# Optimization experiments

Hardware: AMD Instinct MI355X
Metric: run time of the kernel (lower is better)

## Reference

```python
import jax, jax.numpy as jnp
import numpy as np

N, E, R, D = 50000, 1600000, 512, 64

def _mlp(x, w1, b1, w2, b2):
    # torch nn.Linear: y = x @ W.T + b ; Sequential(Linear(2D,D), ReLU, Linear(D,D))
    h = jax.nn.relu(x @ w1.T + b1)
    return h @ w2.T + b2

def setup_inputs() -> dict:
    key = jax.random.key(0)
    ks = jax.random.split(key, 8)
    edge_index = jax.random.randint(ks[0], (2, E), 0, N, dtype=jnp.int64)
    edge_type = jax.random.randint(ks[1], (E,), 0, R, dtype=jnp.int64)
    rel = jax.random.normal(ks[2], (R, D), dtype=jnp.float32)
    s2d = 1.0 / np.sqrt(2.0 * D)
    sd = 1.0 / np.sqrt(1.0 * D)
    w1a = jax.random.normal(ks[3], (D, 2 * D), dtype=jnp.float32) * s2d
    w2a = jax.random.normal(ks[4], (D, D), dtype=jnp.float32) * sd
    w1b = jax.random.normal(ks[5], (D, 2 * D), dtype=jnp.float32) * s2d
    w2b = jax.random.normal(ks[6], (D, D), dtype=jnp.float32) * sd
    zeros = jnp.zeros((D,), jnp.float32)
    strength = jnp.full((1,), 0.1, dtype=jnp.float32)
    return {
        'edge_index': edge_index, 'edge_type': edge_type,
        'relation_embeddings': rel,
        'w1a': w1a, 'b1a': zeros, 'w2a': w2a, 'b2a': zeros,
        'w1b': w1b, 'b1b': zeros, 'w2b': w2b, 'b2b': zeros,
        'strength': strength, 'num_nodes': N,
    }

def reference(edge_index, edge_type, relation_embeddings,
              w1a, b1a, w2a, b2a, w1b, b1b, w2b, b2b,
              strength, num_nodes):
    # Batched version of compute_entity_relation_features over all entities.
    # For entity e: feat = mean of relation embeddings over edges incident to e
    # (each edge counted once, as in the boolean-mask original).
    src, dst = edge_index[0], edge_index[1]
    rel_e = relation_embeddings[edge_type]                      # [E, D]
    not_self = (src != dst).astype(rel_e.dtype)                 # avoid double-count self-loops
    sum_feat = (jax.ops.segment_sum(rel_e, src, num_segments=num_nodes)
                + jax.ops.segment_sum(rel_e * not_self[:, None], dst, num_segments=num_nodes))
    ones = jnp.ones((rel_e.shape[0],), rel_e.dtype)
    deg = (jax.ops.segment_sum(ones, src, num_segments=num_nodes)
           + jax.ops.segment_sum(not_self, dst, num_segments=num_nodes))  # [N]
    has_edge = deg > 0
    rel_ctx = relation_embeddings.mean(axis=0)                  # [D]
    feat = jnp.where(has_edge[:, None], sum_feat / jnp.maximum(deg, 1.0)[:, None], rel_ctx)

    # interaction branch: cat(feat, global relation context) -> MLP a
    ctx_b = jnp.broadcast_to(rel_ctx, feat.shape)
    interaction = _mlp(jnp.concatenate([feat, ctx_b], axis=-1), w1a, b1a, w2a, b2a)
    # context branch: neighbor_context == entity_relation_avg == feat
    ctx_feat_n = _mlp(jnp.concatenate([feat, feat], axis=-1), w1b, b1b, w2b, b2b)
    # has_neighbor: at least one non-self-loop incident edge
    nbr_deg = (jax.ops.segment_sum(not_self, src, num_segments=num_nodes)
               + jax.ops.segment_sum(not_self, dst, num_segments=num_nodes))
    has_nbr = nbr_deg > 0
    context_feat = jnp.where(has_nbr[:, None], ctx_feat_n, interaction)

    s = jnp.clip(strength[0], 0.0, 0.3)
    enhanced = (1.0 - s) * feat + s * context_feat
    # entities with no incident edges fall back to mean relation embedding
    return jnp.where(has_edge[:, None], enhanced, rel_ctx)
```

## Files before the change

### kernel.cpp

```cpp
#include <hip/hip_runtime.h>

#define DD   64
#define WSH  6
#define WSZ  64
#define TILE 4096
#define ALGN 16
#define GMAX 1024
#define SMAX 1024
#define CAP  8192
#define LSTG 20480
#define RK   512

typedef unsigned int u32;
typedef unsigned short u16;
typedef __attribute__((ext_vector_type(4))) float f32x4;
typedef __attribute__((ext_vector_type(4))) u32 u32x4;
typedef __attribute__((ext_vector_type(8))) short short8;


__device__ inline u32 f2bf(float x) {
    u32 u = __float_as_uint(x);
    return (u + 0x7FFFu + ((u >> 16) & 1u)) >> 16;
}
__device__ inline float bf2f(u32 b) { return __uint_as_float(b << 16); }
__device__ inline int swz16(int row, int col) {
    return row * 64 + ((((col >> 3) ^ (row & 7)) << 3) | (col & 7));
}
__device__ inline u32 pack_bf_hi(float lo, float hi) {
    return __builtin_amdgcn_perm(__float_as_uint(hi), __float_as_uint(lo),
                                 0x07060302u);
}

__global__ __launch_bounds__(512)
void k_prep(const float* __restrict__ rel, int R, float* __restrict__ ctxpart,
            u16* __restrict__ relT, const float* __restrict__ w1,
            const float* __restrict__ w2, u16* __restrict__ w1t,
            u16* __restrict__ w2t, int* __restrict__ gcur, int G) {
    if (blockIdx.x == 8) {
        for (int i = threadIdx.x; i < DD * DD; i += 512) {
            int j = i >> 6, k = i & 63;
            w1t[i] = (u16)f2bf(w1[j * 2 * DD + k] + w1[j * 2 * DD + DD + k]);
            w2t[i] = (u16)f2bf(w2[i]);
        }
        for (int i = threadIdx.x; i < G + 1; i += 512) gcur[i] = 0;
        return;
    }
    __shared__ float part[8][DD];
    int k0 = blockIdx.x * (RK / 8);
    int d  = threadIdx.x & 63;
    int rg = threadIdx.x >> 6;
    float s = 0.f;
    #pragma unroll
    for (int i = 0; i < 8; ++i) {
        int k = k0 + rg * 8 + i;
        float v = rel[k * DD + d];
        relT[d * RK + k] = (u16)f2bf(v);
        s += v;
    }
    part[rg][d] = s;
    __syncthreads();
    if (threadIdx.x < DD) {
        float t = 0.f;
        #pragma unroll
        for (int i = 0; i < 8; ++i) t += part[i][threadIdx.x];
        ctxpart[blockIdx.x * DD + threadIdx.x] = t;
    }
}

__global__ __launch_bounds__(512)
void k_gplace(const int* __restrict__ src, const int* __restrict__ dst,
              const int* __restrict__ etype, int* __restrict__ gcur,
              u16* __restrict__ es, u32* __restrict__ selflist,
              int* __restrict__ slcnt, int E, int G) {
    __shared__ int lcnt[GMAX];
    __shared__ int lbase[GMAX];
    __shared__ int loff[GMAX];
    __shared__ int lcur[GMAX];
    __shared__ __align__(32) u16 stage[LSTG];
    int tid = threadIdx.x;
    for (int i = tid; i < GMAX; i += 512) lcnt[i] = 0;
    __syncthreads();
    int t0 = blockIdx.x * TILE;
    int t1 = min(t0 + TILE, E);
    for (int i = t0 + tid; i < t1; i += 512) {
        int s = src[i], d = dst[i];
        atomicAdd(&lcnt[s >> WSH], 1);
        if (s != d) atomicAdd(&lcnt[d >> WSH], 1);
    }
    __syncthreads();
    for (int i = tid; i < GMAX; i += 512)
        loff[i] = (i < G) ? ((lcnt[i] + ALGN - 1) & ~(ALGN - 1)) : 0;
    __syncthreads();
    for (int d2 = 1; d2 < GMAX; d2 <<= 1) {
        int v0 = (tid >= d2) ? loff[tid - d2] : 0;
        int v1 = loff[tid + 512 - d2];
        __syncthreads();
        loff[tid] += v0;
        loff[tid + 512] += v1;
        __syncthreads();
    }
    for (int g = tid; g < G; g += 512) {
        int c = lcnt[g];
        int pad = (c + ALGN - 1) & ~(ALGN - 1);
        int st = loff[g] - pad;
        loff[g] = st;
        lcur[g] = st;
        lbase[g] = c ? atomicAdd(&gcur[g], pad) : 0;
    }
    __syncthreads();
    for (int i = t0 + tid; i < t1; i += 512) {
        int s = src[i], d = dst[i];
        u32 t = (u32)etype[i];
        int gs = s >> WSH;
        int p = atomicAdd(&lcur[gs], 1);
        stage[p] = (u16)((u32)(s & 63) | (t << 6));
        if (s != d) {
            int gd = d >> WSH;
            int q = atomicAdd(&lcur[gd], 1);
            stage[q] = (u16)((u32)(d & 63) | (t << 6));
        } else {
            int p2 = atomicAdd(slcnt, 1);
            if (p2 < SMAX) selflist[p2] = ((u32)s << 9) | t;
        }
    }
    __syncthreads();
    for (int g = tid; g < G; g += 512) {
        int c = lcnt[g];
        if (!c) continue;
        int pad = (c + ALGN - 1) & ~(ALGN - 1);
        int st = loff[g];
        for (int p = st + c; p < st + pad; ++p) stage[p] = 0xFFFFu;
    }
    __syncthreads();
    for (int g = tid; g < G; g += 512) {
        int c = lcnt[g];
        if (!c) continue;
        int pad = (c + ALGN - 1) & ~(ALGN - 1);
        int st = loff[g];
        int gb = lbase[g];
        u16* dp = es + (size_t)g * CAP + gb;
        for (int off = 0; off < pad; off += 16) {
            if (gb + off + 16 <= CAP) {
                u32x4 a = *(const u32x4*)(stage + st + off);
                u32x4 b = *(const u32x4*)(stage + st + off + 8);
                *(u32x4*)(dp + off) = a;
                *(u32x4*)(dp + off + 8) = b;
            }
        }
    }
}

__global__ __launch_bounds__(512, 2)
void k_win(const u16* __restrict__ es, const int* __restrict__ gcur,
           const u16* __restrict__ relT, const u16* __restrict__ w1t,
           const u16* __restrict__ w2t, const float* __restrict__ ctxpart,
           int R, const float* __restrict__ b1, const float* __restrict__ b2,
           const float* __restrict__ strength, float* __restrict__ out,
           const u32* __restrict__ selflist, const int* __restrict__ slcnt,
           const float* __restrict__ w1a, const float* __restrict__ b1a,
           const float* __restrict__ w2a, const float* __restrict__ b2a,
           int N, int GW) {
    __shared__ __align__(16) u32 Hn[WSZ * RK / 8];
    __shared__ __align__(16) u16 rt[2][WSZ * DD];
    __shared__ __align__(16) u16 w1s[DD * DD];
    __shared__ __align__(16) u16 w2s[DD * DD];
    __shared__ __align__(16) u16 Fb[WSZ * DD];
    __shared__ int cnts[WSZ];
    __shared__ int selfc[WSZ];
    __shared__ float invd[WSZ];
    __shared__ float b1s[DD], b2s[DD], ctx_s[DD];
    u16* H1b = (u16*)Hn;

    int tid = threadIdx.x;
    int lane = tid & 63;
    int wv = tid >> 6;
    int scol = tid >> 3, skk = (tid & 7) * 8;

    if (tid < DD) {
        b1s[tid] = b1[tid]; b2s[tid] = b2[tid];
        float t = 0.f;
        #pragma unroll
        for (int i = 0; i < 8; ++i) t += ctxpart[i * DD + tid];
        ctx_s[tid] = t / (float)R;
    }
    {
        short8 wv1 = *(const short8*)(w1t + scol * DD + skk);
        short8 wv2 = *(const short8*)(w2t + scol * DD + skk);
        *(short8*)(w1s + swz16(scol, skk)) = wv1;
        *(short8*)(w2s + swz16(scol, skk)) = wv2;
    }
    float sc = fminf(fmaxf(strength[0], 0.f), 0.3f);
    int scount = min(*slcnt, SMAX);

    int mb = wv >> 1;
    int nb0 = (wv & 1) * 2;
    int arow = mb * 16 + (lane & 15);
    int kgrp = (lane >> 4) * 8;
    int col0 = nb0 * 16 + (lane & 15);
    int col1 = col0 + 16;

    for (int w = blockIdx.x; w < GW; w += gridDim.x) {
        __syncthreads();
        for (int i = tid; i < WSZ * RK / 8; i += 512) Hn[i] = 0;
        if (tid < WSZ) selfc[tid] = 0;
        int cntE = min(gcur[w], CAP);
        short8 stg0 = *(const short8*)(relT + scol * RK + skk);
        __syncthreads();

        const u32x4* es128 = (const u32x4*)(es + (size_t)w * CAP);
        int nv = cntE >> 3;
        for (int i = tid; i < nv; i += 512) {
            u32x4 v4 = es128[i];
            #pragma unroll
            for (int c = 0; c < 4; ++c) {
                u32 v2 = v4[c];
                #pragma unroll
                for (int h = 0; h < 2; ++h) {
                    u32 v = h ? (v2 >> 16) : (v2 & 0xFFFFu);
                    if (v == 0xFFFFu) continue;
                    int r = (int)(v & 63);
                    int t = (int)((v >> 6) & 0x1FF);
                    int word = r * 64 + ((t >> 3) ^ ((r & 7) << 2));
                    atomicAdd(&Hn[word], 1u << ((t & 7) * 4));
                }
            }
        }
        for (int i = tid; i < scount; i += 512) {
            int n = (int)(selflist[i] >> 9);
            if ((n >> WSH) == w) atomicAdd(&selfc[n & 63], 1);
        }
        __syncthreads();
        {
            int row = tid >> 3;
            int s = 0;
            int w0 = row * 64 + (tid & 7) * 8;
            #pragma unroll
            for (int i = 0; i < 8; ++i) {
                u32 v = Hn[w0 + i];
                u32 a = (v & 0x0F0F0F0Fu) + ((v >> 4) & 0x0F0F0F0Fu);
                s += (int)((a & 0xFF) + ((a >> 8) & 0xFF) +
                           ((a >> 16) & 0xFF) + (a >> 24));
            }
            s += __shfl_down(s, 4); s += __shfl_down(s, 2); s += __shfl_down(s, 1);
            if ((tid & 7) == 0) cnts[row] = s;
        }
        *(short8*)(rt[0] + swz16(scol, skk)) = stg0;
        __syncthreads();
        if (tid < WSZ) {
            int c = cnts[tid];
            invd[tid] = c ? 1.f / (float)c : 0.f;
        }
        u32 aw[16];
        {
            int abase = arow * 64;
            int kg = kgrp >> 3;
            #pragma unroll
            for (int ks = 0; ks < 16; ++ks)
                aw[ks] = Hn[abase + ((ks * 4 + kg) ^ ((arow & 7) << 2))];
        }
        __syncthreads();

        f32x4 acc0 = {0.f, 0.f, 0.f, 0.f}, acc1 = {0.f, 0.f, 0.f, 0.f};
        #pragma unroll
        for (int q = 0; q < 8; ++q) {
            short8 nxt;
            if (q < 7)
                nxt = *(const short8*)(relT + scol * RK + (q + 1) * 64 + skk);
            const u16* rb = rt[q & 1];
            #pragma unroll
            for (int s2 = 0; s2 < 2; ++s2) {
                int koff = s2 * 32 + kgrp;
                u32 v = aw[q * 2 + s2];
                u32 af32[4];
                #pragma unroll
                for (int e = 0; e < 4; ++e) {
                    float g0 = (float)((v >> (8 * e)) & 0xFu);
                    float g1 = (float)((v >> (8 * e + 4)) & 0xFu);
                    af32[e] = pack_bf_hi(g0, g1);
                }
                short8 af = *(short8*)af32;
                const short8* bp0 = (const short8*)
                    (rb + col0 * 64 + (((koff >> 3) ^ (col0 & 7)) << 3));
                const short8* bp1 = (const short8*)
                    (rb + col1 * 64 + (((koff >> 3) ^ (col1 & 7)) << 3));
                acc0 = __builtin_amdgcn_mfma_f32_16x16x32_bf16(af, *bp0, acc0, 0, 0, 0);
                acc1 = __builtin_amdgcn_mfma_f32_16x16x32_bf16(af, *bp1, acc1, 0, 0, 0);
            }
            if (q < 7) {
                __syncthreads();
                *(short8*)(rt[(q + 1) & 1] + swz16(scol, skk)) = nxt;
                __syncthreads();
            }
        }
        __syncthreads();
        #pragma unroll
        for (int r = 0; r < 4; ++r) {
            int row = mb * 16 + (lane >> 4) * 4 + r;
            float iv = invd[row];
            Fb[swz16(row, col0)] = (u16)f2bf(acc0[r] * iv);
            Fb[swz16(row, col1)] = (u16)f2bf(acc1[r] * iv);
        }
        __syncthreads();

        f32x4 ac20 = {0.f, 0.f, 0.f, 0.f}, ac21 = {0.f, 0.f, 0.f, 0.f};
        #pragma unroll
        for (int ks = 0; ks < 2; ++ks) {
            int kb = ks * 32 + kgrp;
            const short8* ap = (const short8*)
                (Fb + arow * 64 + (((kb >> 3) ^ (arow & 7)) << 3));
            const short8* bp0 = (const short8*)
                (w1s + col0 * 64 + (((kb >> 3) ^ (col0 & 7)) << 3));
            const short8* bp1 = (const short8*)
                (w1s + col1 * 64 + (((kb >> 3) ^ (col1 & 7)) << 3));
            ac20 = __builtin_amdgcn_mfma_f32_16x16x32_bf16(*ap, *bp0, ac20, 0, 0, 0);
            ac21 = __builtin_amdgcn_mfma_f32_16x16x32_bf16(*ap, *bp1, ac21, 0, 0, 0);
        }
        __syncthreads();
        #pragma unroll
        for (int r = 0; r < 4; ++r) {
            int row = mb * 16 + (lane >> 4) * 4 + r;
            H1b[swz16(row, col0)] = (u16)f2bf(fmaxf(ac20[r] + b1s[col0], 0.f));
            H1b[swz16(row, col1)] = (u16)f2bf(fmaxf(ac21[r] + b1s[col1], 0.f));
        }
        __syncthreads();

        f32x4 ac30 = {0.f, 0.f, 0.f, 0.f}, ac31 = {0.f, 0.f, 0.f, 0.f};
        #pragma unroll
        for (int ks = 0; ks < 2; ++ks) {
            int kb = ks * 32 + kgrp;
            const short8* ap = (const short8*)
                (H1b + arow * 64 + (((kb >> 3) ^ (arow & 7)) << 3));
            const short8* bp0 = (const short8*)
                (w2s + col0 * 64 + (((kb >> 3) ^ (col0 & 7)) << 3));
            const short8* bp1 = (const short8*)
                (w2s + col1 * 64 + (((kb >> 3) ^ (col1 & 7)) << 3));
            ac30 = __builtin_amdgcn_mfma_f32_16x16x32_bf16(*ap, *bp0, ac30, 0, 0, 0);
            ac31 = __builtin_amdgcn_mfma_f32_16x16x32_bf16(*ap, *bp1, ac31, 0, 0, 0);
        }
        #pragma unroll
        for (int r = 0; r < 4; ++r) {
            int row = mb * 16 + (lane >> 4) * 4 + r;
            int n = (w << WSH) + row;
            if (n >= N) continue;
            int c = cnts[row];
            if (c > 0 && selfc[row] == c) continue;
            #pragma unroll
            for (int q = 0; q < 2; ++q) {
                int col = (nb0 + q) * 16 + (lane & 15);
                float o = (q == 0 ? ac30[r] : ac31[r]) + b2s[col];
                float f = bf2f(Fb[swz16(row, col)]);
                out[n * DD + col] = (c == 0) ? ctx_s[col] : (1.f - sc) * f + sc * o;
            }
        }
        if (wv == 0) {
            bool fl;
            {
                int c = cnts[lane];
                fl = (c > 0) && (selfc[lane] == c) && ((w << WSH) + lane < N);
            }
            unsigned long long m = __ballot(fl);
            float cx = ctx_s[lane];
            while (m) {
                int rr = __ffsll(m) - 1;
                m &= m - 1;
                int n = (w << WSH) + rr;
                float f = bf2f(Fb[swz16(rr, lane)]);
                float h = b1a[lane];
                for (int k = 0; k < DD; ++k)
                    h = fmaf(__shfl(f, k), w1a[lane * 2 * DD + k], h);
                for (int k = 0; k < DD; ++k)
                    h = fmaf(__shfl(cx, k), w1a[lane * 2 * DD + DD + k], h);
                h = fmaxf(h, 0.f);
                float o = b2a[lane];
                for (int k = 0; k < DD; ++k)
                    o = fmaf(__shfl(h, k), w2a[lane * DD + k], o);
                out[n * DD + lane] = (1.f - sc) * f + sc * o;
            }
        }
    }
}

extern "C" void kernel_launch(void* const* d_in, const int* in_sizes, int n_in,
                              void* d_out, int out_size, void* d_ws, size_t ws_size,
                              hipStream_t stream) {
    const int*   edge_index = (const int*)d_in[0];
    const int*   etype      = (const int*)d_in[1];
    const float* rel        = (const float*)d_in[2];
    const float* w1a        = (const float*)d_in[3];
    const float* b1a        = (const float*)d_in[4];
    const float* w2a        = (const float*)d_in[5];
    const float* b2a        = (const float*)d_in[6];
    const float* w1b        = (const float*)d_in[7];
    const float* b1b        = (const float*)d_in[8];
    const float* w2b        = (const float*)d_in[9];
    const float* b2b        = (const float*)d_in[10];
    const float* strength   = (const float*)d_in[11];

    int E = in_sizes[0] / 2;
    int R = in_sizes[2] / DD;
    int N = out_size / DD;
    int GW = (N + WSZ - 1) >> WSH;

    float* out = (float*)d_out;
    char*  p   = (char*)d_ws;

    int*   gcur    = (int*)p;   p += (size_t)GW * sizeof(int);
    int*   slcnt   = (int*)p;   p += sizeof(int);
    float* ctxpart = (float*)p; p += 8 * DD * sizeof(float);
    p = (char*)(((size_t)p + 15) & ~(size_t)15);
    u16*   relT     = (u16*)p; p += (size_t)RK * DD * sizeof(u16);
    u16*   w1t      = (u16*)p; p += (size_t)DD * DD * sizeof(u16);
    u16*   w2t      = (u16*)p; p += (size_t)DD * DD * sizeof(u16);
    u32*   selflist = (u32*)p; p += (size_t)SMAX * sizeof(u32);
    u16*   es       = (u16*)p;

    k_prep<<<9, 512, 0, stream>>>(rel, R, ctxpart, relT, w1b, w2b, w1t, w2t,
                                  gcur, GW);

    const int* src = edge_index;
    const int* dst = edge_index + E;
    int nb = (E + TILE - 1) / TILE;

    k_gplace<<<nb, 512, 0, stream>>>(src, dst, etype, gcur, es,
                                     selflist, slcnt, E, GW);

    int nwb = (GW + 1) / 2;
    k_win<<<nwb, 512, 0, stream>>>(es, gcur, relT, w1t, w2t, ctxpart, R,
                                   b1b, b2b, strength, out,
                                   selflist, slcnt, w1a, b1a, w2a, b2a, N, GW);
}
```

Before: 63.63 us.

## Keep relation table resident in LDS, use 1024-thread persistent blocks with edge prefetch

The window kernel now loads the whole transposed relation table once per block into padded LDS. This replaces the double-buffered per-window streaming that needed two barriers per K-step. Blocks grow to 1024 threads (16 waves, one 16x16 output tile each), the grid becomes a fixed 256 persistent blocks, and each thread prefetches its edge vector for the next window during the current one. The trade is higher LDS use per block and lower block-level occupancy in exchange for fewer syncs and fewer global reloads.

After: 60.55 us. 4.8% less time.

```diff
diff --git a/kernel.cpp b/kernel.cpp
--- a/kernel.cpp
+++ b/kernel.cpp
@@ -10,6 +10,8 @@
 #define CAP  8192
 #define LSTG 20480
 #define RK   512
+#define RTP  520
+#define NWB  256
 
 typedef unsigned int u32;
 typedef unsigned short u16;
@@ -150,7 +152,7 @@
     }
 }
 
-__global__ __launch_bounds__(512, 2)
+__global__ __launch_bounds__(1024, 1)
 void k_win(const u16* __restrict__ es, const int* __restrict__ gcur,
            const u16* __restrict__ relT, const u16* __restrict__ w1t,
            const u16* __restrict__ w2t, const float* __restrict__ ctxpart,
@@ -161,21 +163,19 @@
            const float* __restrict__ w2a, const float* __restrict__ b2a,
            int N, int GW) {
     __shared__ __align__(16) u32 Hn[WSZ * RK / 8];
-    __shared__ __align__(16) u16 rt[2][WSZ * DD];
+    __shared__ __align__(16) u16 rt[WSZ * RTP];
     __shared__ __align__(16) u16 w1s[DD * DD];
     __shared__ __align__(16) u16 w2s[DD * DD];
-    __shared__ __align__(16) u16 Fb[WSZ * DD];
+    __shared__ __align__(16) u16 Fb[DD * DD];
+    __shared__ __align__(16) u16 H1b[DD * DD];
     __shared__ int cnts[WSZ];
     __shared__ int selfc[WSZ];
     __shared__ float invd[WSZ];
     __shared__ float b1s[DD], b2s[DD], ctx_s[DD];
-    u16* H1b = (u16*)Hn;
 
     int tid = threadIdx.x;
     int lane = tid & 63;
     int wv = tid >> 6;
-    int scol = tid >> 3, skk = (tid & 7) * 8;
-
     if (tid < DD) {
         b1s[tid] = b1[tid]; b2s[tid] = b2[tid];
         float t = 0.f;
@@ -183,37 +183,44 @@
         for (int i = 0; i < 8; ++i) t += ctxpart[i * DD + tid];
         ctx_s[tid] = t / (float)R;
     }
-    {
-        short8 wv1 = *(const short8*)(w1t + scol * DD + skk);
-        short8 wv2 = *(const short8*)(w2t + scol * DD + skk);
-        *(short8*)(w1s + swz16(scol, skk)) = wv1;
-        *(short8*)(w2s + swz16(scol, skk)) = wv2;
+    for (int i = tid; i < 4096; i += 1024) {
+        int col = i >> 6, k8 = i & 63;
+        *(short8*)(rt + col * RTP + k8 * 8) =
+            *(const short8*)(relT + col * RK + k8 * 8);
+    }
+    if (tid < 512) {
+        int col = tid >> 3, kk = (tid & 7) * 8;
+        *(short8*)(w1s + swz16(col, kk)) = *(const short8*)(w1t + col * DD + kk);
+        *(short8*)(w2s + swz16(col, kk)) = *(const short8*)(w2t + col * DD + kk);
     }
     float sc = fminf(fmaxf(strength[0], 0.f), 0.3f);
     int scount = min(*slcnt, SMAX);
 
-    int mb = wv >> 1;
-    int nb0 = (wv & 1) * 2;
+    int mb = wv >> 2, nbq = wv & 3;
     int arow = mb * 16 + (lane & 15);
     int kgrp = (lane >> 4) * 8;
-    int col0 = nb0 * 16 + (lane & 15);
-    int col1 = col0 + 16;
-
-    for (int w = blockIdx.x; w < GW; w += gridDim.x) {
-        __syncthreads();
-        for (int i = tid; i < WSZ * RK / 8; i += 512) Hn[i] = 0;
+    int kg = kgrp >> 3;
+    int col = nbq * 16 + (lane & 15);
+
+    int w = blockIdx.x;
+    u32x4 myv = {0u, 0u, 0u, 0u};
+    bool have = false;
+    if (w < GW) {
+        int cntE = min(gcur[w], CAP);
+        int nv = cntE >> 3;
+        if (tid < nv) { myv = ((const u32x4*)(es + (size_t)w * CAP))[tid]; have = true; }
+    }
+
+    for (; w < GW; ) {
+        int wn = w + gridDim.x;
+        __syncthreads();
+        for (int i = tid; i < 4096; i += 1024) Hn[i] = 0;
         if (tid < WSZ) selfc[tid] = 0;
-        int cntE = min(gcur[w], CAP);
-        short8 stg0 = *(const short8*)(relT + scol * RK + skk);
-        __syncthreads();
-
-        const u32x4* es128 = (const u32x4*)(es + (size_t)w * CAP);
-        int nv = cntE >> 3;
-        for (int i = tid; i < nv; i += 512) {
-            u32x4 v4 = es128[i];
+        __syncthreads();
+        if (have) {
             #pragma unroll
             for (int c = 0; c < 4; ++c) {
-                u32 v2 = v4[c];
+                u32 v2 = myv[c];
                 #pragma unroll
                 for (int h = 0; h < 2; ++h) {
                     u32 v = h ? (v2 >> 16) : (v2 & 0xFFFFu);
@@ -225,12 +232,18 @@
                 }
             }
         }
-        for (int i = tid; i < scount; i += 512) {
+        for (int i = tid; i < scount; i += 1024) {
             int n = (int)(selflist[i] >> 9);
             if ((n >> WSH) == w) atomicAdd(&selfc[n & 63], 1);
         }
-        __syncthreads();
-        {
+        u32x4 nxtv = {0u, 0u, 0u, 0u};
+        bool haven = false;
+        if (wn < GW) {
+            int cn = min(gcur[wn], CAP) >> 3;
+            if (tid < cn) { nxtv = ((const u32x4*)(es + (size_t)wn * CAP))[tid]; haven = true; }
+        }
+        __syncthreads();
+        if (tid < 512) {
             int row = tid >> 3;
             int s = 0;
             int w0 = row * 64 + (tid & 7) * 8;
@@ -242,100 +255,66 @@
                            ((a >> 16) & 0xFF) + (a >> 24));
             }
             s += __shfl_down(s, 4); s += __shfl_down(s, 2); s += __shfl_down(s, 1);
-            if ((tid & 7) == 0) cnts[row] = s;
-        }
-        *(short8*)(rt[0] + swz16(scol, skk)) = stg0;
-        __syncthreads();
-        if (tid < WSZ) {
-            int c = cnts[tid];
-            invd[tid] = c ? 1.f / (float)c : 0.f;
-        }
+            if ((tid & 7) == 0) { cnts[row] = s; invd[row] = s ? 1.f / s : 0.f; }
+        }
+        __syncthreads();
+
         u32 aw[16];
         {
             int abase = arow * 64;
-            int kg = kgrp >> 3;
             #pragma unroll
             for (int ks = 0; ks < 16; ++ks)
                 aw[ks] = Hn[abase + ((ks * 4 + kg) ^ ((arow & 7) << 2))];
         }
-        __syncthreads();
-
-        f32x4 acc0 = {0.f, 0.f, 0.f, 0.f}, acc1 = {0.f, 0.f, 0.f, 0.f};
-        #pragma unroll
-        for (int q = 0; q < 8; ++q) {
-            short8 nxt;
-            if (q < 7)
-                nxt = *(const short8*)(relT + scol * RK + (q + 1) * 64 + skk);
-            const u16* rb = rt[q & 1];
+        f32x4 acc = {0.f, 0.f, 0.f, 0.f};
+        #pragma unroll
+        for (int q = 0; q < 16; ++q) {
+            int k8 = (q * 32 + kgrp) >> 3;
+            u32 v = aw[q];
+            u32 af32[4];
             #pragma unroll
-            for (int s2 = 0; s2 < 2; ++s2) {
-                int koff = s2 * 32 + kgrp;
-                u32 v = aw[q * 2 + s2];
-                u32 af32[4];
-                #pragma unroll
-                for (int e = 0; e < 4; ++e) {
-                    float g0 = (float)((v >> (8 * e)) & 0xFu);
-                    float g1 = (float)((v >> (8 * e + 4)) & 0xFu);
-                    af32[e] = pack_bf_hi(g0, g1);
-                }
-                short8 af = *(short8*)af32;
-                const short8* bp0 = (const short8*)
-                    (rb + col0 * 64 + (((koff >> 3) ^ (col0 & 7)) << 3));
-                const short8* bp1 = (const short8*)
-                    (rb + col1 * 64 + (((koff >> 3) ^ (col1 & 7)) << 3));
-                acc0 = __builtin_amdgcn_mfma_f32_16x16x32_bf16(af, *bp0, acc0, 0, 0, 0);
-                acc1 = __builtin_amdgcn_mfma_f32_16x16x32_bf16(af, *bp1, acc1, 0, 0, 0);
+            for (int e = 0; e < 4; ++e) {
+                float g0 = (float)((v >> (8 * e)) & 0xFu);
+                float g1 = (float)((v >> (8 * e + 4)) & 0xFu);
+                af32[e] = pack_bf_hi(g0, g1);
             }
-            if (q < 7) {
-                __syncthreads();
-                *(short8*)(rt[(q + 1) & 1] + swz16(scol, skk)) = nxt;
-                __syncthreads();
-            }
-        }
-        __syncthreads();
+            short8 af = *(short8*)af32;
+            const short8* bp = (const short8*)(rt + col * RTP + k8 * 8);
+            acc = __builtin_amdgcn_mfma_f32_16x16x32_bf16(af, *bp, acc, 0, 0, 0);
+        }
         #pragma unroll
         for (int r = 0; r < 4; ++r) {
             int row = mb * 16 + (lane >> 4) * 4 + r;
-            float iv = invd[row];
-            Fb[swz16(row, col0)] = (u16)f2bf(acc0[r] * iv);
-            Fb[swz16(row, col1)] = (u16)f2bf(acc1[r] * iv);
-        }
-        __syncthreads();
-
-        f32x4 ac20 = {0.f, 0.f, 0.f, 0.f}, ac21 = {0.f, 0.f, 0.f, 0.f};
+            Fb[swz16(row, col)] = (u16)f2bf(acc[r] * invd[row]);
+        }
+        __syncthreads();
+
+        f32x4 a2 = {0.f, 0.f, 0.f, 0.f};
         #pragma unroll
         for (int ks = 0; ks < 2; ++ks) {
             int kb = ks * 32 + kgrp;
             const short8* ap = (const short8*)
                 (Fb + arow * 64 + (((kb >> 3) ^ (arow & 7)) << 3));
-            const short8* bp0 = (const short8*)
-                (w1s + col0 * 64 + (((kb >> 3) ^ (col0 & 7)) << 3));
-            const short8* bp1 = (const short8*)
-                (w1s + col1 * 64 + (((kb >> 3) ^ (col1 & 7)) << 3));
-            ac20 = __builtin_amdgcn_mfma_f32_16x16x32_bf16(*ap, *bp0, ac20, 0, 0, 0);
-            ac21 = __builtin_amdgcn_mfma_f32_16x16x32_bf16(*ap, *bp1, ac21, 0, 0, 0);
-        }
-        __syncthreads();
+            const short8* bp = (const short8*)
+                (w1s + col * 64 + (((kb >> 3) ^ (col & 7)) << 3));
+            a2 = __builtin_amdgcn_mfma_f32_16x16x32_bf16(*ap, *bp, a2, 0, 0, 0);
+        }
         #pragma unroll
         for (int r = 0; r < 4; ++r) {
             int row = mb * 16 + (lane >> 4) * 4 + r;
-            H1b[swz16(row, col0)] = (u16)f2bf(fmaxf(ac20[r] + b1s[col0], 0.f));
-            H1b[swz16(row, col1)] = (u16)f2bf(fmaxf(ac21[r] + b1s[col1], 0.f));
-        }
-        __syncthreads();
-
-        f32x4 ac30 = {0.f, 0.f, 0.f, 0.f}, ac31 = {0.f, 0.f, 0.f, 0.f};
+            H1b[swz16(row, col)] = (u16)f2bf(fmaxf(a2[r] + b1s[col], 0.f));
+        }
+        __syncthreads();
+
+        f32x4 a3 = {0.f, 0.f, 0.f, 0.f};
         #pragma unroll
         for (int ks = 0; ks < 2; ++ks) {
             int kb = ks * 32 + kgrp;
             const short8* ap = (const short8*)
                 (H1b + arow * 64 + (((kb >> 3) ^ (arow & 7)) << 3));
-            const short8* bp0 = (const short8*)
-                (w2s + col0 * 64 + (((kb >> 3) ^ (col0 & 7)) << 3));
-            const short8* bp1 = (const short8*)
-                (w2s + col1 * 64 + (((kb >> 3) ^ (col1 & 7)) << 3));
-            ac30 = __builtin_amdgcn_mfma_f32_16x16x32_bf16(*ap, *bp0, ac30, 0, 0, 0);
-            ac31 = __builtin_amdgcn_mfma_f32_16x16x32_bf16(*ap, *bp1, ac31, 0, 0, 0);
+            const short8* bp = (const short8*)
+                (w2s + col * 64 + (((kb >> 3) ^ (col & 7)) << 3));
+            a3 = __builtin_amdgcn_mfma_f32_16x16x32_bf16(*ap, *bp, a3, 0, 0, 0);
         }
         #pragma unroll
         for (int r = 0; r < 4; ++r) {
@@ -344,20 +323,13 @@
             if (n >= N) continue;
             int c = cnts[row];
             if (c > 0 && selfc[row] == c) continue;
-            #pragma unroll
-            for (int q = 0; q < 2; ++q) {
-                int col = (nb0 + q) * 16 + (lane & 15);
-                float o = (q == 0 ? ac30[r] : ac31[r]) + b2s[col];
-                float f = bf2f(Fb[swz16(row, col)]);
-                out[n * DD + col] = (c == 0) ? ctx_s[col] : (1.f - sc) * f + sc * o;
-            }
+            float o = a3[r] + b2s[col];
+            float f = bf2f(Fb[swz16(row, col)]);
+            out[n * DD + col] = (c == 0) ? ctx_s[col] : (1.f - sc) * f + sc * o;
         }
         if (wv == 0) {
-            bool fl;
-            {
-                int c = cnts[lane];
-                fl = (c > 0) && (selfc[lane] == c) && ((w << WSH) + lane < N);
-            }
+            int c = cnts[lane];
+            bool fl = (c > 0) && (selfc[lane] == c) && ((w << WSH) + lane < N);
             unsigned long long m = __ballot(fl);
             float cx = ctx_s[lane];
             while (m) {
@@ -377,6 +349,7 @@
                 out[n * DD + lane] = (1.f - sc) * f + sc * o;
             }
         }
+        myv = nxtv; have = haven; w = wn;
     }
 }
 
@@ -424,8 +397,8 @@
     k_gplace<<<nb, 512, 0, stream>>>(src, dst, etype, gcur, es,
                                      selflist, slcnt, E, GW);
 
-    int nwb = (GW + 1) / 2;
-    k_win<<<nwb, 512, 0, stream>>>(es, gcur, relT, w1t, w2t, ctxpart, R,
-                                   b1b, b2b, strength, out,
-                                   selflist, slcnt, w1a, b1a, w2a, b2a, N, GW);
-}
+    k_win<<<NWB, 1024, 0, stream>>>(es, gcur, relT, w1t, w2t, ctxpart, R,
+                                    b1b, b2b, strength, out,
+                                    selflist, slcnt, w1a, b1a, w2a, b2a,
+                                    N, GW);
+}
```
